# Kernel optimization log

Hardware: AMD Instinct MI355X
Metric: run time of the kernel (lower is better)

The kernel has to match this reference:

```python
import jax, jax.numpy as jnp
import numpy as np

B, S, H, E, I = 2, 1024, 1024, 8, 512
EPS = 1e-8  # torch F.cosine_similarity eps


def setup_inputs() -> dict:
    key = jax.random.key(0)
    ks = jax.random.split(key, 5)
    return {
        "hidden_states": jax.random.normal(ks[0], (B, S, H), dtype=jnp.float32),
        "expert_embeddings": jax.random.normal(ks[1], (E, H), dtype=jnp.float32),
        # torch init is zeros; -0.03 keeps the zero-selection fallback (which NaNs the
        # original's softmax) from ever triggering while preserving ~half-dense routing
        "gate_threshold": jnp.full((E,), -0.03, dtype=jnp.float32),
        "w_gate": jax.random.normal(ks[2], (E, H, I), dtype=jnp.float32) / np.sqrt(H).astype(np.float32),
        "w_up": jax.random.normal(ks[3], (E, H, I), dtype=jnp.float32) / np.sqrt(H).astype(np.float32),
        "w_down": jax.random.normal(ks[4], (E, I, H), dtype=jnp.float32) / np.sqrt(I).astype(np.float32),
    }


def _forward(hidden_states, expert_embeddings, gate_threshold, w_gate, w_up, w_down):
    b, s, h = hidden_states.shape
    n_experts = expert_embeddings.shape[0]
    x = hidden_states.reshape(-1, h)  # [T, H]

    # cosine-similarity routing scores [T, E]
    xn = x / jnp.maximum(jnp.linalg.norm(x, axis=-1, keepdims=True), EPS)
    en = expert_embeddings / jnp.maximum(jnp.linalg.norm(expert_embeddings, axis=-1, keepdims=True), EPS)
    scores = xn @ en.T

    # SiLUHardThreshold forward: hard 0/1 mask (used only as a boolean downstream,
    # so no gradient flows through it in the module's output path)
    routing_mask = (jax.nn.silu(scores - gate_threshold) > 0).astype(scores.dtype)

    # guarantee at least one expert per token: fall back to top-1 score
    num_sel = routing_mask.sum(axis=-1)  # [T]
    top1 = jnp.argmax(scores, axis=-1)   # [T]
    routing_mask_final = jnp.where((num_sel == 0)[:, None],
                                   jax.nn.one_hot(top1, n_experts, dtype=scores.dtype),
                                   routing_mask)

    # softmax over selected experts (pre-fallback mask, as in the original)
    masked_scores = jnp.where(routing_mask > 0, scores, -jnp.inf)
    routing_weights = jax.nn.softmax(masked_scores.astype(jnp.float32), axis=-1).astype(x.dtype)
    gates = routing_weights * routing_mask_final  # [T, E] combine weights

    # per-expert Qwen3 SwiGLU MLP: down(silu(gate(x)) * up(x)); dense over experts,
    # gated combine is the vectorized equivalent of the gather/MLP/index_add loop
    hmid = jax.nn.silu(jnp.einsum('th,ehi->eti', x, w_gate)) * jnp.einsum('th,ehi->eti', x, w_up)  # [E,T,I]
    out = jnp.einsum('eti,eih,te->th', hmid, w_down, gates)  # [T, H]

    return out.reshape(b, s, h), scores


def reference(hidden_states, expert_embeddings, gate_threshold, w_gate, w_up, w_down):
    # returns (final_hidden_states [B,S,H], router_logits [T,E])
    return _forward(hidden_states, expert_embeddings, gate_threshold, w_gate, w_up, w_down)
```

## Files before the change

kernel.cpp:

```cpp
#include <hip/hip_runtime.h>
#include <hip/hip_bf16.h>
#include <stdint.h>

#define T_TOK 2048
#define H_DIM 1024
#define E_NUM 8
#define I_DIM 512
#define KDOWN (E_NUM * I_DIM)
#define EPSR 1e-8f

typedef short s16x8 __attribute__((ext_vector_type(8)));
typedef float f32x4 __attribute__((ext_vector_type(4)));

static __device__ __forceinline__ uint16_t f2bf(float f) {
    union { float f; uint32_t i; } v; v.f = f;
    uint32_t lsb = (v.i >> 16) & 1u;
    v.i += 0x7fffu + lsb;
    return (uint16_t)(v.i >> 16);
}

static __device__ __forceinline__ void gll16(const void* g, void* l) {
    __builtin_amdgcn_global_load_lds(
        (const __attribute__((address_space(1))) void*)g,
        (__attribute__((address_space(3))) void*)l, 16, 0, 0);
}

__global__ __launch_bounds__(256) void transpose_all_kernel(
    const float* __restrict__ wg, const float* __restrict__ wu,
    const float* __restrict__ wd, uint16_t* __restrict__ wgT,
    uint16_t* __restrict__ wuT, uint16_t* __restrict__ wdT) {
    __shared__ float tile[64][68];
    const int z = blockIdx.z;
    const float* src; uint16_t* dst; int C, out_stride, r0, c0;
    if (z < 16) {
        const int e = z & 7;
        src = (z < 8 ? wg : wu) + (long)e * H_DIM * I_DIM;
        dst = (z < 8 ? wgT : wuT) + (long)e * I_DIM * H_DIM;
        C = I_DIM; out_stride = H_DIM;
        r0 = blockIdx.y * 64; c0 = blockIdx.x * 64;
    } else {
        const int e = z - 16;
        src = wd + (long)e * I_DIM * H_DIM;
        dst = wdT + (long)e * I_DIM;
        C = H_DIM; out_stride = KDOWN;
        r0 = blockIdx.x * 64; c0 = blockIdx.y * 64;
    }
    const int tid = threadIdx.x;
    const int g16 = tid >> 4, l16 = (tid & 15) * 4;
    #pragma unroll
    for (int it = 0; it < 4; ++it) {
        int r = it * 16 + g16;
        *(float4*)&tile[r][l16] = *(const float4*)(src + (long)(r0 + r) * C + c0 + l16);
    }
    __syncthreads();
    #pragma unroll
    for (int it = 0; it < 4; ++it) {
        int oc = it * 16 + g16;
        ushort4 o;
        o.x = f2bf(tile[l16 + 0][oc]);
        o.y = f2bf(tile[l16 + 1][oc]);
        o.z = f2bf(tile[l16 + 2][oc]);
        o.w = f2bf(tile[l16 + 3][oc]);
        *(ushort4*)(dst + (long)(c0 + oc) * out_stride + r0 + l16) = o;
    }
}

__global__ __launch_bounds__(256) void routing_kernel(
    const float* __restrict__ x, const float* __restrict__ emb,
    const float* __restrict__ thr, float* __restrict__ scores_out,
    float* __restrict__ gates, uint16_t* __restrict__ xb) {
    __shared__ float semb[E_NUM * H_DIM];
    __shared__ float senorm[E_NUM];
    const int tid = threadIdx.x;
    const int lane = tid & 63;
    const int wave = tid >> 6;
    for (int i = tid; i < E_NUM * H_DIM; i += 256) semb[i] = emb[i];
    __syncthreads();
    for (int e = wave; e < E_NUM; e += 4) {
        float s = 0.f;
        #pragma unroll
        for (int c = 0; c < 16; ++c) { float v = semb[e * H_DIM + lane + 64 * c]; s += v * v; }
        #pragma unroll
        for (int off = 32; off; off >>= 1) s += __shfl_xor(s, off);
        if (lane == 0) senorm[e] = fmaxf(sqrtf(s), EPSR);
    }
    __syncthreads();
    const int t = blockIdx.x * 4 + wave;
    const float* xt = x + (long)t * H_DIM;
    uint16_t* xbt = xb + (long)t * H_DIM;
    float nrm = 0.f, dot[E_NUM];
    #pragma unroll
    for (int e = 0; e < E_NUM; ++e) dot[e] = 0.f;
    #pragma unroll
    for (int c = 0; c < 16; ++c) {
        float v = xt[lane + 64 * c];
        xbt[lane + 64 * c] = f2bf(v);
        nrm += v * v;
        #pragma unroll
        for (int e = 0; e < E_NUM; ++e) dot[e] += v * semb[e * H_DIM + lane + 64 * c];
    }
    #pragma unroll
    for (int off = 32; off; off >>= 1) {
        nrm += __shfl_xor(nrm, off);
        #pragma unroll
        for (int e = 0; e < E_NUM; ++e) dot[e] += __shfl_xor(dot[e], off);
    }
    float xn = fmaxf(sqrtf(nrm), EPSR);
    float sc[E_NUM], sel[E_NUM];
    float msel = -1e30f, mall = -1e30f;
    int nsel = 0, arg = 0;
    #pragma unroll
    for (int e = 0; e < E_NUM; ++e) {
        sc[e] = dot[e] / (xn * senorm[e]);
        float d = sc[e] - thr[e];
        sel[e] = (d > 0.f) ? 1.f : 0.f;
        if (d > 0.f) { nsel++; msel = fmaxf(msel, sc[e]); }
        if (sc[e] > mall) { mall = sc[e]; arg = e; }
    }
    float w[E_NUM], den = 0.f;
    #pragma unroll
    for (int e = 0; e < E_NUM; ++e) { w[e] = (sel[e] > 0.f) ? __expf(sc[e] - msel) : 0.f; den += w[e]; }
    if (lane == 0) {
        #pragma unroll
        for (int e = 0; e < E_NUM; ++e) {
            scores_out[t * E_NUM + e] = sc[e];
            gates[t * E_NUM + e] = (nsel > 0) ? (w[e] / den) : ((e == arg) ? 1.f : 0.f);
        }
    }
}

__global__ __launch_bounds__(256, 2) void moe_gateup_kernel(
    const uint16_t* __restrict__ xb,
    const uint16_t* __restrict__ wgT,
    const uint16_t* __restrict__ wuT,
    const float* __restrict__ gates,
    uint16_t* __restrict__ hmid) {
    const int e  = blockIdx.z;
    const int t0 = blockIdx.x * 256;
    const int i0 = blockIdx.y * 64;
    __shared__ uint16_t sG[2][64][64];
    __shared__ uint16_t sU[2][64][64];
    __shared__ float sGate[256];
    const int tid  = threadIdx.x;
    const int lane = tid & 63;
    const int wave = tid >> 6;
    sGate[tid] = gates[(t0 + tid) * E_NUM + e];

    const int srow = wave * 16 + (lane >> 3);
    const int scol = ((lane & 7) ^ (srow & 7)) * 8;
    const uint16_t* gg = wgT + ((long)e * I_DIM + i0 + srow) * H_DIM + scol;
    const uint16_t* gu = wuT + ((long)e * I_DIM + i0 + srow) * H_DIM + scol;

    const int q = lane >> 4, r16 = lane & 15;
    const int sw = r16 & 7;
    const uint16_t* ax = xb + (long)(t0 + wave * 64 + r16) * H_DIM + q * 8;

    f32x4 accg[4][4] = {}, accu[4][4] = {};

    #pragma unroll
    for (int j = 0; j < 2; ++j) {
        gll16(gg + (long)j * 8 * H_DIM, &sG[0][wave * 16 + j * 8][0]);
        gll16(gu + (long)j * 8 * H_DIM, &sU[0][wave * 16 + j * 8][0]);
    }
    __syncthreads();

    for (int it = 0; it < 16; ++it) {
        const int kb = it * 64;
        const int b = it & 1;
        s16x8 af[2][4];
        #pragma unroll
        for (int kk = 0; kk < 2; ++kk)
            #pragma unroll
            for (int m = 0; m < 4; ++m)
                af[kk][m] = *(const s16x8*)(ax + (long)m * 16 * H_DIM + kb + kk * 32);
        if (it < 15) {
            #pragma unroll
            for (int j = 0; j < 2; ++j) {
                gll16(gg + (long)j * 8 * H_DIM + kb + 64, &sG[b ^ 1][wave * 16 + j * 8][0]);
                gll16(gu + (long)j * 8 * H_DIM + kb + 64, &sU[b ^ 1][wave * 16 + j * 8][0]);
            }
        }
        #pragma unroll
        for (int kk = 0; kk < 2; ++kk) {
            const int pc = ((kk * 4 + q) ^ sw) * 8;
            s16x8 gf[4], uf[4];
            #pragma unroll
            for (int n = 0; n < 4; ++n) {
                gf[n] = *(const s16x8*)&sG[b][n * 16 + r16][pc];
                uf[n] = *(const s16x8*)&sU[b][n * 16 + r16][pc];
            }
            #pragma unroll
            for (int m = 0; m < 4; ++m)
                #pragma unroll
                for (int n = 0; n < 4; ++n) {
                    accg[m][n] = __builtin_amdgcn_mfma_f32_16x16x32_bf16(af[kk][m], gf[n], accg[m][n], 0, 0, 0);
                    accu[m][n] = __builtin_amdgcn_mfma_f32_16x16x32_bf16(af[kk][m], uf[n], accu[m][n], 0, 0, 0);
                }
        }
        __syncthreads();
    }
    #pragma unroll
    for (int m = 0; m < 4; ++m) {
        #pragma unroll
        for (int rr = 0; rr < 4; ++rr) {
            const int trow = wave * 64 + m * 16 + q * 4 + rr;
            const float gate = sGate[trow];
            const long base = (long)(t0 + trow) * KDOWN + e * I_DIM + i0;
            #pragma unroll
            for (int n = 0; n < 4; ++n) {
                float g = accg[m][n][rr], u = accu[m][n][rr];
                float h = gate * (g / (1.f + __expf(-g))) * u;
                hmid[base + n * 16 + r16] = f2bf(h);
            }
        }
    }
}

__global__ __launch_bounds__(256, 3) void moe_down_kernel(
    const uint16_t* __restrict__ hmid,
    const uint16_t* __restrict__ wdT,
    float* __restrict__ out,
    float* __restrict__ parts) {
    const int t0 = blockIdx.x * 256;
    const int h0 = blockIdx.y * 64;
    const int kz = blockIdx.z;
    const int it0 = (kz < 4) ? kz * 11 : 44 + (kz - 4) * 10;
    const int nit = (kz < 4) ? 11 : 10;
    __shared__ uint16_t sB[2][64][64];
    const int tid  = threadIdx.x;
    const int lane = tid & 63;
    const int wave = tid >> 6;

    const int srow = wave * 16 + (lane >> 3);
    const int scol = ((lane & 7) ^ (srow & 7)) * 8;
    const uint16_t* gb = wdT + ((long)h0 + srow) * KDOWN + scol;

    const int q = lane >> 4, r16 = lane & 15;
    const int sw = r16 & 7;
    const uint16_t* ax = hmid + (long)(t0 + wave * 64 + r16) * KDOWN + q * 8;

    f32x4 acc[4][4] = {};

    #pragma unroll
    for (int j = 0; j < 2; ++j)
        gll16(gb + (long)it0 * 64 + (long)j * 8 * KDOWN, &sB[0][wave * 16 + j * 8][0]);
    __syncthreads();

    for (int it = 0; it < nit; ++it) {
        const int kb = (it0 + it) * 64;
        const int b = it & 1;
        s16x8 af[2][4];
        #pragma unroll
        for (int kk = 0; kk < 2; ++kk)
            #pragma unroll
            for (int m = 0; m < 4; ++m)
                af[kk][m] = *(const s16x8*)(ax + (long)m * 16 * KDOWN + kb + kk * 32);
        if (it + 1 < nit) {
            #pragma unroll
            for (int j = 0; j < 2; ++j)
                gll16(gb + (long)(kb + 64) + (long)j * 8 * KDOWN, &sB[b ^ 1][wave * 16 + j * 8][0]);
        }
        #pragma unroll
        for (int kk = 0; kk < 2; ++kk) {
            const int pc = ((kk * 4 + q) ^ sw) * 8;
            s16x8 bf[4];
            #pragma unroll
            for (int n = 0; n < 4; ++n)
                bf[n] = *(const s16x8*)&sB[b][n * 16 + r16][pc];
            #pragma unroll
            for (int m = 0; m < 4; ++m)
                #pragma unroll
                for (int n = 0; n < 4; ++n)
                    acc[m][n] = __builtin_amdgcn_mfma_f32_16x16x32_bf16(af[kk][m], bf[n], acc[m][n], 0, 0, 0);
        }
        __syncthreads();
    }
    float* dst = (kz == 0) ? out : (parts + (long)(kz - 1) * T_TOK * H_DIM);
    #pragma unroll
    for (int m = 0; m < 4; ++m) {
        #pragma unroll
        for (int rr = 0; rr < 4; ++rr) {
            const int t = t0 + wave * 64 + m * 16 + q * 4 + rr;
            #pragma unroll
            for (int n = 0; n < 4; ++n)
                dst[(long)t * H_DIM + h0 + n * 16 + r16] = acc[m][n][rr];
        }
    }
}

__global__ __launch_bounds__(256) void reduce_kernel(float* __restrict__ out,
                                                     const float* __restrict__ parts) {
    long i = ((long)blockIdx.x * 256 + threadIdx.x) * 4;
    float4 a = *(const float4*)(out + i);
    #pragma unroll
    for (int j = 0; j < 5; ++j) {
        float4 b = *(const float4*)(parts + (long)j * T_TOK * H_DIM + i);
        a.x += b.x; a.y += b.y; a.z += b.z; a.w += b.w;
    }
    *(float4*)(out + i) = a;
}

extern "C" void kernel_launch(void* const* d_in, const int* in_sizes, int n_in,
                              void* d_out, int out_size, void* d_ws, size_t ws_size,
                              hipStream_t stream) {
    const float* x    = (const float*)d_in[0];
    const float* emb  = (const float*)d_in[1];
    const float* thr  = (const float*)d_in[2];
    const float* wg   = (const float*)d_in[3];
    const float* wu   = (const float*)d_in[4];
    const float* wd   = (const float*)d_in[5];
    float* out    = (float*)d_out;
    float* scores = out + (size_t)T_TOK * H_DIM;

    uint8_t* ws = (uint8_t*)d_ws;
    uint16_t* xb   = (uint16_t*)(ws);
    uint16_t* wgT  = (uint16_t*)(ws + (size_t)4  * 1048576);
    uint16_t* wuT  = (uint16_t*)(ws + (size_t)12 * 1048576);
    uint16_t* wdT  = (uint16_t*)(ws + (size_t)20 * 1048576);
    uint16_t* hmid = (uint16_t*)(ws + (size_t)28 * 1048576);
    float*    gates = (float*)  (ws + (size_t)44 * 1048576);
    float*    parts = (float*)  (ws + (size_t)48 * 1048576);

    transpose_all_kernel<<<dim3(8, 16, 24), 256, 0, stream>>>(wg, wu, wd, wgT, wuT, wdT);
    routing_kernel<<<T_TOK / 4, 256, 0, stream>>>(x, emb, thr, scores, gates, xb);
    moe_gateup_kernel<<<dim3(T_TOK / 256, I_DIM / 64, E_NUM), 256, 0, stream>>>(
        xb, wgT, wuT, gates, hmid);
    moe_down_kernel<<<dim3(T_TOK / 256, H_DIM / 64, 6), 256, 0, stream>>>(hmid, wdT, out, parts);
    reduce_kernel<<<(T_TOK * H_DIM) / 1024, 256, 0, stream>>>(out, parts);
}
```

Measured before the change: 210.5 us.

## Stage activations in LDS with 2x2 wave tiling for gate-up and down GEMMs

Both expert GEMM kernels change from each wave streaming its own 64 token rows directly from global memory to a 128x128 block tile. A and B tiles are both staged in LDS through global_load_lds, and the four waves are arranged 2x2 so each A fragment is shared across two waves. The double-buffered prefetch is dropped in favour of a simple two-barrier single-buffer loop. The down kernel's split-K goes from 6 uneven chunks to 4 equal ones, so the reduce kernel sums fewer partial buffers. This gives better operand reuse and less global traffic, at the cost of exposed load latency and more barriers per iteration.

```diff
diff --git a/kernel.cpp b/kernel.cpp
--- a/kernel.cpp
+++ b/kernel.cpp
@@ -136,81 +136,71 @@
     const float* __restrict__ gates,
     uint16_t* __restrict__ hmid) {
     const int e  = blockIdx.z;
-    const int t0 = blockIdx.x * 256;
-    const int i0 = blockIdx.y * 64;
-    __shared__ uint16_t sG[2][64][64];
-    __shared__ uint16_t sU[2][64][64];
-    __shared__ float sGate[256];
+    const int t0 = blockIdx.x * 128;
+    const int i0 = blockIdx.y * 128;
+    __shared__ uint16_t sA[128][64];
+    __shared__ uint16_t sG[128][64];
+    __shared__ uint16_t sU[128][64];
+    __shared__ float sGate[128];
     const int tid  = threadIdx.x;
     const int lane = tid & 63;
     const int wave = tid >> 6;
-    sGate[tid] = gates[(t0 + tid) * E_NUM + e];
-
-    const int srow = wave * 16 + (lane >> 3);
+    const int wm = wave >> 1, wn = wave & 1;
+    if (tid < 128) sGate[tid] = gates[(t0 + tid) * E_NUM + e];
+
+    const int srow = wave * 32 + (lane >> 3);
     const int scol = ((lane & 7) ^ (srow & 7)) * 8;
+    const uint16_t* ga = xb  + (long)(t0 + srow) * H_DIM + scol;
     const uint16_t* gg = wgT + ((long)e * I_DIM + i0 + srow) * H_DIM + scol;
     const uint16_t* gu = wuT + ((long)e * I_DIM + i0 + srow) * H_DIM + scol;
 
+    f32x4 accg[4][4] = {}, accu[4][4] = {};
     const int q = lane >> 4, r16 = lane & 15;
     const int sw = r16 & 7;
-    const uint16_t* ax = xb + (long)(t0 + wave * 64 + r16) * H_DIM + q * 8;
-
-    f32x4 accg[4][4] = {}, accu[4][4] = {};
-
-    #pragma unroll
-    for (int j = 0; j < 2; ++j) {
-        gll16(gg + (long)j * 8 * H_DIM, &sG[0][wave * 16 + j * 8][0]);
-        gll16(gu + (long)j * 8 * H_DIM, &sU[0][wave * 16 + j * 8][0]);
-    }
-    __syncthreads();
-
-    for (int it = 0; it < 16; ++it) {
-        const int kb = it * 64;
-        const int b = it & 1;
-        s16x8 af[2][4];
-        #pragma unroll
-        for (int kk = 0; kk < 2; ++kk)
-            #pragma unroll
-            for (int m = 0; m < 4; ++m)
-                af[kk][m] = *(const s16x8*)(ax + (long)m * 16 * H_DIM + kb + kk * 32);
-        if (it < 15) {
-            #pragma unroll
-            for (int j = 0; j < 2; ++j) {
-                gll16(gg + (long)j * 8 * H_DIM + kb + 64, &sG[b ^ 1][wave * 16 + j * 8][0]);
-                gll16(gu + (long)j * 8 * H_DIM + kb + 64, &sU[b ^ 1][wave * 16 + j * 8][0]);
-            }
-        }
+
+    for (int kb = 0; kb < H_DIM; kb += 64) {
+        __syncthreads();
+        #pragma unroll
+        for (int j = 0; j < 4; ++j) {
+            const int lr = wave * 32 + j * 8;
+            gll16(ga + (long)j * 8 * H_DIM + kb, &sA[lr][0]);
+            gll16(gg + (long)j * 8 * H_DIM + kb, &sG[lr][0]);
+            gll16(gu + (long)j * 8 * H_DIM + kb, &sU[lr][0]);
+        }
+        __syncthreads();
         #pragma unroll
         for (int kk = 0; kk < 2; ++kk) {
             const int pc = ((kk * 4 + q) ^ sw) * 8;
-            s16x8 gf[4], uf[4];
+            s16x8 af[4], gf[4], uf[4];
+            #pragma unroll
+            for (int m = 0; m < 4; ++m)
+                af[m] = *(const s16x8*)&sA[wm * 64 + m * 16 + r16][pc];
             #pragma unroll
             for (int n = 0; n < 4; ++n) {
-                gf[n] = *(const s16x8*)&sG[b][n * 16 + r16][pc];
-                uf[n] = *(const s16x8*)&sU[b][n * 16 + r16][pc];
+                gf[n] = *(const s16x8*)&sG[wn * 64 + n * 16 + r16][pc];
+                uf[n] = *(const s16x8*)&sU[wn * 64 + n * 16 + r16][pc];
             }
             #pragma unroll
             for (int m = 0; m < 4; ++m)
                 #pragma unroll
                 for (int n = 0; n < 4; ++n) {
-                    accg[m][n] = __builtin_amdgcn_mfma_f32_16x16x32_bf16(af[kk][m], gf[n], accg[m][n], 0, 0, 0);
-                    accu[m][n] = __builtin_amdgcn_mfma_f32_16x16x32_bf16(af[kk][m], uf[n], accu[m][n], 0, 0, 0);
+                    accg[m][n] = __builtin_amdgcn_mfma_f32_16x16x32_bf16(af[m], gf[n], accg[m][n], 0, 0, 0);
+                    accu[m][n] = __builtin_amdgcn_mfma_f32_16x16x32_bf16(af[m], uf[n], accu[m][n], 0, 0, 0);
                 }
         }
-        __syncthreads();
     }
     #pragma unroll
     for (int m = 0; m < 4; ++m) {
         #pragma unroll
         for (int rr = 0; rr < 4; ++rr) {
-            const int trow = wave * 64 + m * 16 + q * 4 + rr;
+            const int trow = wm * 64 + m * 16 + q * 4 + rr;
             const float gate = sGate[trow];
             const long base = (long)(t0 + trow) * KDOWN + e * I_DIM + i0;
             #pragma unroll
             for (int n = 0; n < 4; ++n) {
                 float g = accg[m][n][rr], u = accu[m][n][rr];
                 float h = gate * (g / (1.f + __expf(-g))) * u;
-                hmid[base + n * 16 + r16] = f2bf(h);
+                hmid[base + wn * 64 + n * 16 + r16] = f2bf(h);
             }
         }
     }
@@ -221,69 +211,61 @@
     const uint16_t* __restrict__ wdT,
     float* __restrict__ out,
     float* __restrict__ parts) {
-    const int t0 = blockIdx.x * 256;
-    const int h0 = blockIdx.y * 64;
+    const int t0 = blockIdx.x * 128;
+    const int h0 = blockIdx.y * 128;
     const int kz = blockIdx.z;
-    const int it0 = (kz < 4) ? kz * 11 : 44 + (kz - 4) * 10;
-    const int nit = (kz < 4) ? 11 : 10;
-    __shared__ uint16_t sB[2][64][64];
+    const int kst = kz * 1024;
+    __shared__ uint16_t sA[128][64];
+    __shared__ uint16_t sB[128][64];
     const int tid  = threadIdx.x;
     const int lane = tid & 63;
     const int wave = tid >> 6;
-
-    const int srow = wave * 16 + (lane >> 3);
+    const int wm = wave >> 1, wn = wave & 1;
+
+    const int srow = wave * 32 + (lane >> 3);
     const int scol = ((lane & 7) ^ (srow & 7)) * 8;
-    const uint16_t* gb = wdT + ((long)h0 + srow) * KDOWN + scol;
-
+    const uint16_t* ga = hmid + (long)(t0 + srow) * KDOWN + scol;
+    const uint16_t* gb = wdT  + (long)(h0 + srow) * KDOWN + scol;
+
+    f32x4 acc[4][4] = {};
     const int q = lane >> 4, r16 = lane & 15;
     const int sw = r16 & 7;
-    const uint16_t* ax = hmid + (long)(t0 + wave * 64 + r16) * KDOWN + q * 8;
-
-    f32x4 acc[4][4] = {};
-
-    #pragma unroll
-    for (int j = 0; j < 2; ++j)
-        gll16(gb + (long)it0 * 64 + (long)j * 8 * KDOWN, &sB[0][wave * 16 + j * 8][0]);
-    __syncthreads();
-
-    for (int it = 0; it < nit; ++it) {
-        const int kb = (it0 + it) * 64;
-        const int b = it & 1;
-        s16x8 af[2][4];
-        #pragma unroll
-        for (int kk = 0; kk < 2; ++kk)
-            #pragma unroll
-            for (int m = 0; m < 4; ++m)
-                af[kk][m] = *(const s16x8*)(ax + (long)m * 16 * KDOWN + kb + kk * 32);
-        if (it + 1 < nit) {
-            #pragma unroll
-            for (int j = 0; j < 2; ++j)
-                gll16(gb + (long)(kb + 64) + (long)j * 8 * KDOWN, &sB[b ^ 1][wave * 16 + j * 8][0]);
-        }
+
+    for (int kb = kst; kb < kst + 1024; kb += 64) {
+        __syncthreads();
+        #pragma unroll
+        for (int j = 0; j < 4; ++j) {
+            const int lr = wave * 32 + j * 8;
+            gll16(ga + (long)j * 8 * KDOWN + kb, &sA[lr][0]);
+            gll16(gb + (long)j * 8 * KDOWN + kb, &sB[lr][0]);
+        }
+        __syncthreads();
         #pragma unroll
         for (int kk = 0; kk < 2; ++kk) {
             const int pc = ((kk * 4 + q) ^ sw) * 8;
-            s16x8 bf[4];
+            s16x8 af[4], bf[4];
+            #pragma unroll
+            for (int m = 0; m < 4; ++m)
+                af[m] = *(const s16x8*)&sA[wm * 64 + m * 16 + r16][pc];
             #pragma unroll
             for (int n = 0; n < 4; ++n)
-                bf[n] = *(const s16x8*)&sB[b][n * 16 + r16][pc];
+                bf[n] = *(const s16x8*)&sB[wn * 64 + n * 16 + r16][pc];
             #pragma unroll
             for (int m = 0; m < 4; ++m)
                 #pragma unroll
                 for (int n = 0; n < 4; ++n)
-                    acc[m][n] = __builtin_amdgcn_mfma_f32_16x16x32_bf16(af[kk][m], bf[n], acc[m][n], 0, 0, 0);
-        }
-        __syncthreads();
+                    acc[m][n] = __builtin_amdgcn_mfma_f32_16x16x32_bf16(af[m], bf[n], acc[m][n], 0, 0, 0);
+        }
     }
     float* dst = (kz == 0) ? out : (parts + (long)(kz - 1) * T_TOK * H_DIM);
     #pragma unroll
     for (int m = 0; m < 4; ++m) {
         #pragma unroll
         for (int rr = 0; rr < 4; ++rr) {
-            const int t = t0 + wave * 64 + m * 16 + q * 4 + rr;
+            const int t = t0 + wm * 64 + m * 16 + q * 4 + rr;
             #pragma unroll
             for (int n = 0; n < 4; ++n)
-                dst[(long)t * H_DIM + h0 + n * 16 + r16] = acc[m][n][rr];
+                dst[(long)t * H_DIM + h0 + wn * 64 + n * 16 + r16] = acc[m][n][rr];
         }
     }
 }
@@ -293,7 +275,7 @@
     long i = ((long)blockIdx.x * 256 + threadIdx.x) * 4;
     float4 a = *(const float4*)(out + i);
     #pragma unroll
-    for (int j = 0; j < 5; ++j) {
+    for (int j = 0; j < 3; ++j) {
         float4 b = *(const float4*)(parts + (long)j * T_TOK * H_DIM + i);
         a.x += b.x; a.y += b.y; a.z += b.z; a.w += b.w;
     }
@@ -323,8 +305,8 @@
 
     transpose_all_kernel<<<dim3(8, 16, 24), 256, 0, stream>>>(wg, wu, wd, wgT, wuT, wdT);
     routing_kernel<<<T_TOK / 4, 256, 0, stream>>>(x, emb, thr, scores, gates, xb);
-    moe_gateup_kernel<<<dim3(T_TOK / 256, I_DIM / 64, E_NUM), 256, 0, stream>>>(
+    moe_gateup_kernel<<<dim3(T_TOK / 128, I_DIM / 128, E_NUM), 256, 0, stream>>>(
         xb, wgT, wuT, gates, hmid);
-    moe_down_kernel<<<dim3(T_TOK / 256, H_DIM / 64, 6), 256, 0, stream>>>(hmid, wdT, out, parts);
+    moe_down_kernel<<<dim3(T_TOK / 128, H_DIM / 128, 4), 256, 0, stream>>>(hmid, wdT, out, parts);
     reduce_kernel<<<(T_TOK * H_DIM) / 1024, 256, 0, stream>>>(out, parts);
 }
```

Result: faster. 178.4 us (-15.3%).
